# Kernel optimization log

Measured on AMD Instinct MI355X. Metric: run time of the kernel, lower is better.

Reference implementation:

```python
import jax, jax.numpy as jnp
import numpy as np

NUM_EMBEDDINGS = 1024
EMBEDDING_DIM = 64
COMMITMENT_COST = 0.25


def setup_inputs() -> dict:
    key = jax.random.key(0)
    kz, kc = jax.random.split(key)
    z = jax.random.normal(kz, (16, 2048, EMBEDDING_DIM), dtype=jnp.float32)
    # nn.Embedding weight init: uniform(-1/K, 1/K)
    codebook = (jax.random.uniform(kc, (NUM_EMBEDDINGS, EMBEDDING_DIM), dtype=jnp.float32) * 2.0 - 1.0) / NUM_EMBEDDINGS
    return {"z": z, "codebook": codebook}


def reference(z, codebook):
    D = codebook.shape[1]
    K = codebook.shape[0]
    flat_z = z.reshape(-1, D)  # [N, D]
    # squared L2 distances: ||z||^2 + ||e||^2 - 2 z.e  -> [N, K]
    distances = (
        jnp.sum(flat_z ** 2, axis=1, keepdims=True)
        + jnp.sum(codebook ** 2, axis=1)
        - 2.0 * jnp.matmul(flat_z, codebook.T)
    )
    encoding_indices = jnp.argmin(distances, axis=1)  # [N]
    quantized = codebook[encoding_indices].reshape(z.shape)

    e_latent_loss = jnp.mean((jax.lax.stop_gradient(quantized) - z) ** 2)
    q_latent_loss = jnp.mean((quantized - jax.lax.stop_gradient(z)) ** 2)
    vq_loss = q_latent_loss + COMMITMENT_COST * e_latent_loss

    # straight-through estimator
    quantized_st = z + jax.lax.stop_gradient(quantized - z)

    # perplexity from codebook usage histogram
    n = encoding_indices.shape[0]
    counts = jnp.zeros((K,), dtype=jnp.float32).at[encoding_indices].add(1.0)
    avg_probs = counts / n
    perplexity = jnp.exp(-jnp.sum(avg_probs * jnp.log(avg_probs + 1e-10)))

    indices_out = encoding_indices.reshape(z.shape[:-1])
    return quantized_st, vq_loss, indices_out, perplexity
```

## Files before the change

### kernel.cpp

```cpp
#include <hip/hip_runtime.h>
#include <math.h>


#define D 64
#define KC 1024
#define MT 2
#define ROWS (MT * 16)

typedef short short8 __attribute__((ext_vector_type(8)));
typedef short short4v __attribute__((ext_vector_type(4)));
typedef float f32x4 __attribute__((ext_vector_type(4)));

__device__ __forceinline__ unsigned short f2bf(float x) {
  unsigned int u = __float_as_uint(x);
  unsigned int r = (u + 0x7fffu + ((u >> 16) & 1u)) >> 16;
  return (unsigned short)r;
}
__device__ __forceinline__ float bf2f(unsigned short h) {
  return __uint_as_float((unsigned int)h << 16);
}

__global__ __launch_bounds__(256) void vq_prep(
    const float* __restrict__ cb, unsigned short* __restrict__ bsplit,
    float* __restrict__ cbn, unsigned int* __restrict__ hist,
    float* __restrict__ loss_acc) {
  const int k = blockIdx.x * 256 + threadIdx.x;
  const float4* e = (const float4*)(cb + (size_t)k * D);
  unsigned short* bp = bsplit + (size_t)k * 128;
  float s0 = 0.f, s1 = 0.f, s2 = 0.f, s3 = 0.f;
#pragma unroll
  for (int i = 0; i < 16; ++i) {
    float4 v = e[i];
    s0 = fmaf(v.x, v.x, s0);
    s1 = fmaf(v.y, v.y, s1);
    s2 = fmaf(v.z, v.z, s2);
    s3 = fmaf(v.w, v.w, s3);
    unsigned short h0 = f2bf(v.x), h1 = f2bf(v.y), h2 = f2bf(v.z), h3 = f2bf(v.w);
    short4v hv = {(short)h0, (short)h1, (short)h2, (short)h3};
    short4v lv = {(short)f2bf(v.x - bf2f(h0)), (short)f2bf(v.y - bf2f(h1)),
                  (short)f2bf(v.z - bf2f(h2)), (short)f2bf(v.w - bf2f(h3))};
    *(short4v*)(bp + i * 4) = hv;
    *(short4v*)(bp + 64 + i * 4) = lv;
  }
  cbn[k] = (s0 + s1) + (s2 + s3);
  hist[k] = 0u;
  if (k == 0) loss_acc[0] = 0.f;
}

__global__ __launch_bounds__(256)
__attribute__((amdgpu_waves_per_eu(4, 4))) void vq_main(
    const float* __restrict__ z, const unsigned short* __restrict__ bsplit,
    const float* __restrict__ cbn, const float* __restrict__ cb,
    float* __restrict__ out_q, float* __restrict__ out_idx,
    unsigned int* __restrict__ hist, float* __restrict__ loss_acc) {
  __shared__ unsigned short Ash[ROWS * 136];
  __shared__ float srzp[ROWS * 16];
  __shared__ float srz[ROWS];
  __shared__ float candd[4][ROWS][17];
  __shared__ int candk[4][ROWS][17];
  __shared__ int skf[ROWS];
  __shared__ float swav[4];

  const int tid = threadIdx.x;
  const int lane = tid & 63;
  const int wav = tid >> 6;
  const int quad = lane >> 4;
  const int col = lane & 15;
  const int rowbase = blockIdx.x * ROWS;

  const float4* z4 = (const float4*)(z + (size_t)rowbase * D);
#pragma unroll
  for (int it = 0; it < ROWS / 16; ++it) {
    int f4 = it * 256 + tid;
    int row = f4 >> 4, c4 = (f4 & 15) * 4;
    float4 v = z4[f4];
    srzp[f4] = ((v.x * v.x + v.y * v.y) + (v.z * v.z + v.w * v.w));
    unsigned short h0 = f2bf(v.x), h1 = f2bf(v.y), h2 = f2bf(v.z), h3 = f2bf(v.w);
    short4v hv = {(short)h0, (short)h1, (short)h2, (short)h3};
    short4v lv = {(short)f2bf(v.x - bf2f(h0)), (short)f2bf(v.y - bf2f(h1)),
                  (short)f2bf(v.z - bf2f(h2)), (short)f2bf(v.w - bf2f(h3))};
    *(short4v*)&Ash[row * 136 + c4] = hv;
    *(short4v*)&Ash[row * 136 + 64 + c4] = lv;
  }
  __syncthreads();
  if (tid < ROWS) {
    float s = 0.f;
#pragma unroll
    for (int i = 0; i < 16; ++i) s += srzp[tid * 16 + i];
    srz[tid] = s;
  }
  __syncthreads();

  float rzv[MT * 4];
#pragma unroll
  for (int mt = 0; mt < MT; ++mt)
#pragma unroll
    for (int reg = 0; reg < 4; ++reg)
      rzv[mt * 4 + reg] = srz[mt * 16 + quad * 4 + reg];

  short8 a[MT][4];
#pragma unroll
  for (int mt = 0; mt < MT; ++mt) {
    const unsigned short* base = &Ash[(mt * 16 + col) * 136 + quad * 8];
    a[mt][0] = *(const short8*)(base + 0);
    a[mt][1] = *(const short8*)(base + 32);
    a[mt][2] = *(const short8*)(base + 64);
    a[mt][3] = *(const short8*)(base + 96);
  }

  float bestd[MT * 4];
  int bestk[MT * 4];
#pragma unroll
  for (int i = 0; i < MT * 4; ++i) {
    bestd[i] = 3.4e38f;
    bestk[i] = 0;
  }

  const int k0 = wav * 256;
  short8 nb0, nb1, nb2, nb3;
  float nen;
  {
    const unsigned short* bb = bsplit + (size_t)(k0 + col) * 128 + quad * 8;
    nb0 = *(const short8*)(bb + 0);
    nb1 = *(const short8*)(bb + 32);
    nb2 = *(const short8*)(bb + 64);
    nb3 = *(const short8*)(bb + 96);
    nen = cbn[k0 + col];
  }
  for (int kt = 0; kt < 16; ++kt) {
    const int mycode = k0 + kt * 16 + col;
    const short8 b0 = nb0, b1 = nb1, b2 = nb2, b3 = nb3;
    const float en = nen;
    if (kt < 15) {
      const unsigned short* nbb =
          bsplit + (size_t)(mycode + 16) * 128 + quad * 8;
      nb0 = *(const short8*)(nbb + 0);
      nb1 = *(const short8*)(nbb + 32);
      nb2 = *(const short8*)(nbb + 64);
      nb3 = *(const short8*)(nbb + 96);
      nen = cbn[mycode + 16];
    }

    f32x4 acc[MT];
#pragma unroll
    for (int mt = 0; mt < MT; ++mt) acc[mt] = {0.f, 0.f, 0.f, 0.f};
#pragma unroll
    for (int mt = 0; mt < MT; ++mt)
      acc[mt] = __builtin_amdgcn_mfma_f32_16x16x32_bf16(a[mt][0], b0, acc[mt], 0, 0, 0);
#pragma unroll
    for (int mt = 0; mt < MT; ++mt)
      acc[mt] = __builtin_amdgcn_mfma_f32_16x16x32_bf16(a[mt][1], b1, acc[mt], 0, 0, 0);
#pragma unroll
    for (int mt = 0; mt < MT; ++mt)
      acc[mt] = __builtin_amdgcn_mfma_f32_16x16x32_bf16(a[mt][2], b0, acc[mt], 0, 0, 0);
#pragma unroll
    for (int mt = 0; mt < MT; ++mt)
      acc[mt] = __builtin_amdgcn_mfma_f32_16x16x32_bf16(a[mt][3], b1, acc[mt], 0, 0, 0);
#pragma unroll
    for (int mt = 0; mt < MT; ++mt)
      acc[mt] = __builtin_amdgcn_mfma_f32_16x16x32_bf16(a[mt][0], b2, acc[mt], 0, 0, 0);
#pragma unroll
    for (int mt = 0; mt < MT; ++mt)
      acc[mt] = __builtin_amdgcn_mfma_f32_16x16x32_bf16(a[mt][1], b3, acc[mt], 0, 0, 0);

#pragma unroll
    for (int mt = 0; mt < MT; ++mt)
#pragma unroll
      for (int reg = 0; reg < 4; ++reg) {
        float dist = fmaf(-2.0f, acc[mt][reg], rzv[mt * 4 + reg] + en);
        int i = mt * 4 + reg;
        bool better = dist < bestd[i];
        bestk[i] = better ? mycode : bestk[i];
        bestd[i] = better ? dist : bestd[i];
      }
  }

#pragma unroll
  for (int mt = 0; mt < MT; ++mt)
#pragma unroll
    for (int reg = 0; reg < 4; ++reg) {
      int row = mt * 16 + quad * 4 + reg;
      candd[wav][row][col] = bestd[mt * 4 + reg];
      candk[wav][row][col] = bestk[mt * 4 + reg];
    }
  __syncthreads();

  if (lane < ROWS / 4) {
    const int row = wav * (ROWS / 4) + lane;
    float bd1 = 3.4e38f, bd2 = 3.4e38f;
    int bk1 = 0x7fffffff, bk2 = 0x7fffffff;
#pragma unroll
    for (int w = 0; w < 4; ++w)
      for (int c = 0; c < 16; ++c) {
        float dv = candd[w][row][c];
        int kv = candk[w][row][c];
        bool b1 = (dv < bd1) || (dv == bd1 && kv < bk1);
        bool b2 = (dv < bd2) || (dv == bd2 && kv < bk2);
        if (b1) {
          bd2 = bd1; bk2 = bk1;
          bd1 = dv; bk1 = kv;
        } else if (b2) {
          bd2 = dv; bk2 = kv;
        }
      }
    if (bd2 - bd1 < 1e-5f) {
      const int grow = rowbase + row;
      const float4* zp = (const float4*)(z + (size_t)grow * D);
      float s0 = 0.f, s1 = 0.f, s2 = 0.f, s3 = 0.f;
#pragma unroll
      for (int i = 0; i < 16; ++i) {
        float4 v = zp[i];
        s0 = fmaf(v.x, v.x, s0);
        s1 = fmaf(v.y, v.y, s1);
        s2 = fmaf(v.z, v.z, s2);
        s3 = fmaf(v.w, v.w, s3);
      }
      const float rzx = (s0 + s1) + (s2 + s3);
      float dx[2];
      int kk[2] = {bk1, bk2};
#pragma unroll
      for (int c = 0; c < 2; ++c) {
        const float4* e4 = (const float4*)(cb + (size_t)kk[c] * D);
        float d0 = 0.f, d1 = 0.f, d2 = 0.f, d3 = 0.f;
#pragma unroll
        for (int i = 0; i < 16; ++i) {
          float4 v = e4[i];
          float4 zv = zp[i];
          d0 = fmaf(zv.x, v.x, d0);
          d1 = fmaf(zv.y, v.y, d1);
          d2 = fmaf(zv.z, v.z, d2);
          d3 = fmaf(zv.w, v.w, d3);
        }
        float dot = (d0 + d1) + (d2 + d3);
        dx[c] = (rzx + cbn[kk[c]]) - 2.0f * dot;
      }
      if ((dx[1] < dx[0]) || (dx[1] == dx[0] && bk2 < bk1)) bk1 = bk2;
    }
    skf[row] = bk1;
    out_idx[rowbase + row] = (float)bk1;
    atomicAdd(&hist[bk1], 1u);
  }
  __syncthreads();

  float lsum = 0.f;
#pragma unroll
  for (int it = 0; it < ROWS / 16; ++it) {
    int f4 = it * 256 + tid;
    int r = f4 >> 4;
    int c4 = (f4 & 15) * 4;
    int bk = skf[r];
    const float4 q = *(const float4*)(cb + (size_t)bk * D + c4);
    const int grow = rowbase + r;
    const float4 zv = *(const float4*)(z + (size_t)grow * D + c4);
    *(float4*)(out_q + (size_t)grow * D + c4) = q;
    float ax = q.x - zv.x, ay = q.y - zv.y, az = q.z - zv.z, aw = q.w - zv.w;
    lsum += ax * ax + ay * ay + az * az + aw * aw;
  }
#pragma unroll
  for (int off = 32; off > 0; off >>= 1) lsum += __shfl_down(lsum, off, 64);
  if (lane == 0) swav[wav] = lsum;
  __syncthreads();
  if (tid == 0) {
    atomicAdd(loss_acc, (swav[0] + swav[1]) + (swav[2] + swav[3]));
  }
}

__global__ __launch_bounds__(1024) void vq_final(
    const unsigned int* __restrict__ hist, const float* __restrict__ loss_acc,
    float* __restrict__ out_loss, float* __restrict__ out_perp, float inv_n,
    float inv_nd) {
  __shared__ float part[16];
  const int t = threadIdx.x;
  const int lane = t & 63;
  const int wav = t >> 6;
  float p = (float)hist[t] * inv_n;
  float v = p * logf(p + 1e-10f);
#pragma unroll
  for (int off = 32; off > 0; off >>= 1) v += __shfl_down(v, off, 64);
  if (lane == 0) part[wav] = v;
  __syncthreads();
  if (t == 0) {
    float s = 0.f;
#pragma unroll
    for (int j = 0; j < 16; ++j) s += part[j];
    *out_perp = expf(-s);
    *out_loss = 1.25f * loss_acc[0] * inv_nd;
  }
}

extern "C" void kernel_launch(void* const* d_in, const int* in_sizes, int n_in,
                              void* d_out, int out_size, void* d_ws,
                              size_t ws_size, hipStream_t stream) {
  (void)n_in;
  (void)out_size;
  (void)ws_size;
  const float* z = (const float*)d_in[0];
  const float* cb = (const float*)d_in[1];
  const int N = in_sizes[0] / D;

  float* out_q = (float*)d_out;
  float* out_loss = (float*)d_out + (size_t)N * D;
  float* out_idx = out_loss + 1;
  float* out_perp = out_idx + N;

  unsigned int* hist = (unsigned int*)d_ws;
  float* loss_acc = (float*)d_ws + 1024;
  float* cbn = (float*)d_ws + 1040;
  unsigned short* bsplit = (unsigned short*)((float*)d_ws + 2064);

  vq_prep<<<dim3(KC / 256), dim3(256), 0, stream>>>(cb, bsplit, cbn, hist,
                                                    loss_acc);
  vq_main<<<dim3(N / ROWS), dim3(256), 0, stream>>>(z, bsplit, cbn, cb, out_q,
                                                    out_idx, hist, loss_acc);
  vq_final<<<dim3(1), dim3(1024), 0, stream>>>(
      hist, loss_acc, out_loss, out_perp, 1.0f / (float)N,
      1.0f / ((float)N * (float)D));
}
```

Measured before the change: 115.9 us.

## Fuse prep, main and final kernels into one with on-the-fly codebook conversion

```diff
diff --git a/kernel.cpp b/kernel.cpp
--- a/kernel.cpp
+++ b/kernel.cpp
@@ -4,7 +4,7 @@
 
 #define D 64
 #define KC 1024
-#define MT 2
+#define MT 4
 #define ROWS (MT * 16)
 
 typedef short short8 __attribute__((ext_vector_type(8)));
@@ -20,39 +20,23 @@
   return __uint_as_float((unsigned int)h << 16);
 }
 
-__global__ __launch_bounds__(256) void vq_prep(
-    const float* __restrict__ cb, unsigned short* __restrict__ bsplit,
-    float* __restrict__ cbn, unsigned int* __restrict__ hist,
-    float* __restrict__ loss_acc) {
-  const int k = blockIdx.x * 256 + threadIdx.x;
-  const float4* e = (const float4*)(cb + (size_t)k * D);
-  unsigned short* bp = bsplit + (size_t)k * 128;
-  float s0 = 0.f, s1 = 0.f, s2 = 0.f, s3 = 0.f;
-#pragma unroll
-  for (int i = 0; i < 16; ++i) {
-    float4 v = e[i];
-    s0 = fmaf(v.x, v.x, s0);
-    s1 = fmaf(v.y, v.y, s1);
-    s2 = fmaf(v.z, v.z, s2);
-    s3 = fmaf(v.w, v.w, s3);
-    unsigned short h0 = f2bf(v.x), h1 = f2bf(v.y), h2 = f2bf(v.z), h3 = f2bf(v.w);
-    short4v hv = {(short)h0, (short)h1, (short)h2, (short)h3};
-    short4v lv = {(short)f2bf(v.x - bf2f(h0)), (short)f2bf(v.y - bf2f(h1)),
-                  (short)f2bf(v.z - bf2f(h2)), (short)f2bf(v.w - bf2f(h3))};
-    *(short4v*)(bp + i * 4) = hv;
-    *(short4v*)(bp + 64 + i * 4) = lv;
-  }
-  cbn[k] = (s0 + s1) + (s2 + s3);
-  hist[k] = 0u;
-  if (k == 0) loss_acc[0] = 0.f;
-}
-
-__global__ __launch_bounds__(256)
-__attribute__((amdgpu_waves_per_eu(4, 4))) void vq_main(
-    const float* __restrict__ z, const unsigned short* __restrict__ bsplit,
-    const float* __restrict__ cbn, const float* __restrict__ cb,
+__device__ __forceinline__ void cvt8(const float4 a, const float4 b,
+                                     short8& hi, short8& lo) {
+  float v[8] = {a.x, a.y, a.z, a.w, b.x, b.y, b.z, b.w};
+#pragma unroll
+  for (int j = 0; j < 8; ++j) {
+    unsigned short h = f2bf(v[j]);
+    hi[j] = (short)h;
+    lo[j] = (short)f2bf(v[j] - bf2f(h));
+  }
+}
+
+__global__ __launch_bounds__(256, 2) void vq_all(
+    const float* __restrict__ z, const float* __restrict__ cb,
     float* __restrict__ out_q, float* __restrict__ out_idx,
-    unsigned int* __restrict__ hist, float* __restrict__ loss_acc) {
+    unsigned int* __restrict__ hist, float* __restrict__ loss_acc,
+    unsigned int* __restrict__ done, float* __restrict__ out_loss,
+    float* __restrict__ out_perp, float inv_n, float inv_nd, int nblocks) {
   __shared__ unsigned short Ash[ROWS * 136];
   __shared__ float srzp[ROWS * 16];
   __shared__ float srz[ROWS];
@@ -60,6 +44,8 @@
   __shared__ int candk[4][ROWS][17];
   __shared__ int skf[ROWS];
   __shared__ float swav[4];
+  __shared__ unsigned int lhist[KC];
+  __shared__ int sdone;
 
   const int tid = threadIdx.x;
   const int lane = tid & 63;
@@ -75,13 +61,16 @@
     int row = f4 >> 4, c4 = (f4 & 15) * 4;
     float4 v = z4[f4];
     srzp[f4] = ((v.x * v.x + v.y * v.y) + (v.z * v.z + v.w * v.w));
-    unsigned short h0 = f2bf(v.x), h1 = f2bf(v.y), h2 = f2bf(v.z), h3 = f2bf(v.w);
+    unsigned short h0 = f2bf(v.x), h1 = f2bf(v.y), h2 = f2bf(v.z),
+                   h3 = f2bf(v.w);
     short4v hv = {(short)h0, (short)h1, (short)h2, (short)h3};
     short4v lv = {(short)f2bf(v.x - bf2f(h0)), (short)f2bf(v.y - bf2f(h1)),
                   (short)f2bf(v.z - bf2f(h2)), (short)f2bf(v.w - bf2f(h3))};
     *(short4v*)&Ash[row * 136 + c4] = hv;
     *(short4v*)&Ash[row * 136 + 64 + c4] = lv;
   }
+#pragma unroll
+  for (int j = 0; j < KC / 256; ++j) lhist[tid + 256 * j] = 0u;
   __syncthreads();
   if (tid < ROWS) {
     float s = 0.f;
@@ -117,29 +106,38 @@
   }
 
   const int k0 = wav * 256;
-  short8 nb0, nb1, nb2, nb3;
-  float nen;
+  float4 nf0, nf1, nf2, nf3;
   {
-    const unsigned short* bb = bsplit + (size_t)(k0 + col) * 128 + quad * 8;
-    nb0 = *(const short8*)(bb + 0);
-    nb1 = *(const short8*)(bb + 32);
-    nb2 = *(const short8*)(bb + 64);
-    nb3 = *(const short8*)(bb + 96);
-    nen = cbn[k0 + col];
+    const float* cbase = cb + (size_t)(k0 + col) * D + quad * 8;
+    nf0 = *(const float4*)(cbase + 0);
+    nf1 = *(const float4*)(cbase + 4);
+    nf2 = *(const float4*)(cbase + 32);
+    nf3 = *(const float4*)(cbase + 36);
   }
   for (int kt = 0; kt < 16; ++kt) {
     const int mycode = k0 + kt * 16 + col;
-    const short8 b0 = nb0, b1 = nb1, b2 = nb2, b3 = nb3;
-    const float en = nen;
+    const float4 f0 = nf0, f1 = nf1, f2 = nf2, f3 = nf3;
     if (kt < 15) {
-      const unsigned short* nbb =
-          bsplit + (size_t)(mycode + 16) * 128 + quad * 8;
-      nb0 = *(const short8*)(nbb + 0);
-      nb1 = *(const short8*)(nbb + 32);
-      nb2 = *(const short8*)(nbb + 64);
-      nb3 = *(const short8*)(nbb + 96);
-      nen = cbn[mycode + 16];
-    }
+      const float* nb = cb + (size_t)(mycode + 16) * D + quad * 8;
+      nf0 = *(const float4*)(nb + 0);
+      nf1 = *(const float4*)(nb + 4);
+      nf2 = *(const float4*)(nb + 32);
+      nf3 = *(const float4*)(nb + 36);
+    }
+    short8 b0, b1, b2, b3;
+    cvt8(f0, f1, b0, b2);
+    cvt8(f2, f3, b1, b3);
+    float p = 0.f;
+    p = fmaf(f0.x, f0.x, p); p = fmaf(f0.y, f0.y, p);
+    p = fmaf(f0.z, f0.z, p); p = fmaf(f0.w, f0.w, p);
+    p = fmaf(f1.x, f1.x, p); p = fmaf(f1.y, f1.y, p);
+    p = fmaf(f1.z, f1.z, p); p = fmaf(f1.w, f1.w, p);
+    p = fmaf(f2.x, f2.x, p); p = fmaf(f2.y, f2.y, p);
+    p = fmaf(f2.z, f2.z, p); p = fmaf(f2.w, f2.w, p);
+    p = fmaf(f3.x, f3.x, p); p = fmaf(f3.y, f3.y, p);
+    p = fmaf(f3.z, f3.z, p); p = fmaf(f3.w, f3.w, p);
+    float q = p + __shfl_xor(p, 16, 64);
+    const float en = q + __shfl_xor(q, 32, 64);
 
     f32x4 acc[MT];
 #pragma unroll
@@ -185,8 +183,8 @@
     }
   __syncthreads();
 
-  if (lane < ROWS / 4) {
-    const int row = wav * (ROWS / 4) + lane;
+  if (lane < 16) {
+    const int row = wav * 16 + lane;
     float bd1 = 3.4e38f, bd2 = 3.4e38f;
     int bk1 = 0x7fffffff, bk2 = 0x7fffffff;
 #pragma unroll
@@ -194,12 +192,12 @@
       for (int c = 0; c < 16; ++c) {
         float dv = candd[w][row][c];
         int kv = candk[w][row][c];
-        bool b1 = (dv < bd1) || (dv == bd1 && kv < bk1);
-        bool b2 = (dv < bd2) || (dv == bd2 && kv < bk2);
-        if (b1) {
+        bool h1 = (dv < bd1) || (dv == bd1 && kv < bk1);
+        bool h2 = (dv < bd2) || (dv == bd2 && kv < bk2);
+        if (h1) {
           bd2 = bd1; bk2 = bk1;
           bd1 = dv; bk1 = kv;
-        } else if (b2) {
+        } else if (h2) {
           bd2 = dv; bk2 = kv;
         }
       }
@@ -222,6 +220,7 @@
       for (int c = 0; c < 2; ++c) {
         const float4* e4 = (const float4*)(cb + (size_t)kk[c] * D);
         float d0 = 0.f, d1 = 0.f, d2 = 0.f, d3 = 0.f;
+        float n0 = 0.f, n1 = 0.f, n2 = 0.f, n3 = 0.f;
 #pragma unroll
         for (int i = 0; i < 16; ++i) {
           float4 v = e4[i];
@@ -230,17 +229,28 @@
           d1 = fmaf(zv.y, v.y, d1);
           d2 = fmaf(zv.z, v.z, d2);
           d3 = fmaf(zv.w, v.w, d3);
+          n0 = fmaf(v.x, v.x, n0);
+          n1 = fmaf(v.y, v.y, n1);
+          n2 = fmaf(v.z, v.z, n2);
+          n3 = fmaf(v.w, v.w, n3);
         }
         float dot = (d0 + d1) + (d2 + d3);
-        dx[c] = (rzx + cbn[kk[c]]) - 2.0f * dot;
+        float en = (n0 + n1) + (n2 + n3);
+        dx[c] = (rzx + en) - 2.0f * dot;
       }
       if ((dx[1] < dx[0]) || (dx[1] == dx[0] && bk2 < bk1)) bk1 = bk2;
     }
     skf[row] = bk1;
     out_idx[rowbase + row] = (float)bk1;
-    atomicAdd(&hist[bk1], 1u);
-  }
-  __syncthreads();
+    atomicAdd(&lhist[bk1], 1u);
+  }
+  __syncthreads();
+
+#pragma unroll
+  for (int j = 0; j < KC / 256; ++j) {
+    unsigned int c = lhist[tid + 256 * j];
+    if (c) atomicAdd(&hist[tid + 256 * j], c);
+  }
 
   float lsum = 0.f;
 #pragma unroll
@@ -249,11 +259,12 @@
     int r = f4 >> 4;
     int c4 = (f4 & 15) * 4;
     int bk = skf[r];
-    const float4 q = *(const float4*)(cb + (size_t)bk * D + c4);
+    const float4 qv = *(const float4*)(cb + (size_t)bk * D + c4);
     const int grow = rowbase + r;
     const float4 zv = *(const float4*)(z + (size_t)grow * D + c4);
-    *(float4*)(out_q + (size_t)grow * D + c4) = q;
-    float ax = q.x - zv.x, ay = q.y - zv.y, az = q.z - zv.z, aw = q.w - zv.w;
+    *(float4*)(out_q + (size_t)grow * D + c4) = qv;
+    float ax = qv.x - zv.x, ay = qv.y - zv.y, az = qv.z - zv.z,
+          aw = qv.w - zv.w;
     lsum += ax * ax + ay * ay + az * az + aw * aw;
   }
 #pragma unroll
@@ -263,28 +274,32 @@
   if (tid == 0) {
     atomicAdd(loss_acc, (swav[0] + swav[1]) + (swav[2] + swav[3]));
   }
-}
-
-__global__ __launch_bounds__(1024) void vq_final(
-    const unsigned int* __restrict__ hist, const float* __restrict__ loss_acc,
-    float* __restrict__ out_loss, float* __restrict__ out_perp, float inv_n,
-    float inv_nd) {
-  __shared__ float part[16];
-  const int t = threadIdx.x;
-  const int lane = t & 63;
-  const int wav = t >> 6;
-  float p = (float)hist[t] * inv_n;
-  float v = p * logf(p + 1e-10f);
-#pragma unroll
-  for (int off = 32; off > 0; off >>= 1) v += __shfl_down(v, off, 64);
-  if (lane == 0) part[wav] = v;
-  __syncthreads();
-  if (t == 0) {
-    float s = 0.f;
-#pragma unroll
-    for (int j = 0; j < 16; ++j) s += part[j];
-    *out_perp = expf(-s);
-    *out_loss = 1.25f * loss_acc[0] * inv_nd;
+
+  __threadfence();
+  if (tid == 0) {
+    unsigned int o = atomicAdd(done, 1u);
+    sdone = (o == (unsigned int)(nblocks - 1)) ? 1 : 0;
+  }
+  __syncthreads();
+  if (sdone) {
+    __threadfence();
+    float v = 0.f;
+#pragma unroll
+    for (int j = 0; j < KC / 256; ++j) {
+      unsigned int c = atomicAdd(&hist[tid + 256 * j], 0u);
+      float pr = (float)c * inv_n;
+      v += pr * logf(pr + 1e-10f);
+    }
+#pragma unroll
+    for (int off = 32; off > 0; off >>= 1) v += __shfl_down(v, off, 64);
+    if (lane == 0) swav[wav] = v;
+    __syncthreads();
+    if (tid == 0) {
+      float s = (swav[0] + swav[1]) + (swav[2] + swav[3]);
+      *out_perp = expf(-s);
+      float lt = atomicAdd(loss_acc, 0.f);
+      *out_loss = 1.25f * lt * inv_nd;
+    }
   }
 }
 
@@ -305,14 +320,12 @@
 
   unsigned int* hist = (unsigned int*)d_ws;
   float* loss_acc = (float*)d_ws + 1024;
-  float* cbn = (float*)d_ws + 1040;
-  unsigned short* bsplit = (unsigned short*)((float*)d_ws + 2064);
-
-  vq_prep<<<dim3(KC / 256), dim3(256), 0, stream>>>(cb, bsplit, cbn, hist,
-                                                    loss_acc);
-  vq_main<<<dim3(N / ROWS), dim3(256), 0, stream>>>(z, bsplit, cbn, cb, out_q,
-                                                    out_idx, hist, loss_acc);
-  vq_final<<<dim3(1), dim3(1024), 0, stream>>>(
-      hist, loss_acc, out_loss, out_perp, 1.0f / (float)N,
-      1.0f / ((float)N * (float)D));
-}
+  unsigned int* done = (unsigned int*)d_ws + 1025;
+
+  hipMemsetAsync(d_ws, 0, 1026 * sizeof(unsigned int), stream);
+
+  const int nblocks = N / ROWS;
+  vq_all<<<dim3(nblocks), dim3(256), 0, stream>>>(
+      z, cb, out_q, out_idx, hist, loss_acc, done, out_loss, out_perp,
+      1.0f / (float)N, 1.0f / ((float)N * (float)D), nblocks);
+}
```

Result: slower. 150.5 us (+29.8%).
